# Optimization experiments

Measured on AMD Instinct MI355X. Metric: run time of the kernel, lower is better.

The kernel has to match this reference:

```python
import jax, jax.numpy as jnp
import numpy as np

NP_, NA_ = 100000, 50000           # paper / author node counts
E_C, E_W, E_B = 200000, 100000, 100000  # cites, writes, written_by edges
IN_DIM, OUT_DIM, H, DK = 256, 256, 8, 32
SLOPE, EPS = 0.2, 1e-5


def leaky(x):
    return jnp.where(x >= 0, x, SLOPE * x)


def seg_softmax(scores, seg, n):
    # softmax over edges grouped by destination node (DGL edge_softmax)
    m = jax.ops.segment_max(scores, seg, num_segments=n)
    e = jnp.exp(scores - m[seg])
    z = jax.ops.segment_sum(e, seg, num_segments=n)
    return e / z[seg]


def setup_inputs() -> dict:
    key = jax.random.key(0)
    k = jax.random.split(key, 14)
    s = 1.0 / np.sqrt(IN_DIM)
    return {
        "h_paper": jax.random.normal(k[0], (NP_, IN_DIM), jnp.float32),
        "h_author": jax.random.normal(k[1], (NA_, IN_DIM), jnp.float32),
        "fc_W": jax.random.normal(k[2], (OUT_DIM, IN_DIM), jnp.float32) * s,
        "fce_W": jax.random.normal(k[3], (OUT_DIM, OUT_DIM), jnp.float32) * s,
        "edge_emb": jax.random.normal(k[4], (3, OUT_DIM), jnp.float32) * 0.1,
        "attn_l": jax.random.normal(k[5], (1, H, DK), jnp.float32) * 0.1,
        "attn_r": jax.random.normal(k[6], (1, H, DK), jnp.float32) * 0.1,
        "attn_e": jax.random.normal(k[7], (1, H, DK), jnp.float32) * 0.1,
        "gamma": jnp.ones((OUT_DIM,), jnp.float32),
        "beta": jnp.zeros((OUT_DIM,), jnp.float32),
        "cites_src": jax.random.randint(k[8], (E_C,), 0, NP_),
        "cites_dst": jax.random.randint(k[9], (E_C,), 0, NP_),
        "writes_src": jax.random.randint(k[10], (E_W,), 0, NA_),
        "writes_dst": jax.random.randint(k[11], (E_W,), 0, NP_),
        "wb_src": jax.random.randint(k[12], (E_B,), 0, NP_),
        "wb_dst": jax.random.randint(k[13], (E_B,), 0, NA_),
    }


def reference(h_paper, h_author, fc_W, fce_W, edge_emb, attn_l, attn_r, attn_e,
              gamma, beta, cites_src, cites_dst, writes_src, writes_dst,
              wb_src, wb_dst):
    # fc projection (dropout = identity at eval)
    hp = (h_paper @ fc_W.T).reshape(-1, H, DK)   # [NP,H,DK]
    ha = (h_author @ fc_W.T).reshape(-1, H, DK)  # [NA,H,DK]
    # relation/edge-type embedding term: [3,H]
    ee = ((edge_emb @ fce_W.T).reshape(-1, H, DK) * attn_e).sum(-1)
    el_p = (hp * attn_l).sum(-1)  # [NP,H]
    er_p = (hp * attn_r).sum(-1)
    el_a = (ha * attn_l).sum(-1)
    er_a = (ha * attn_r).sum(-1)
    # per-edge unnormalized attention, leaky_relu(u_add_v + edge term)
    a_c = leaky(el_p[cites_src] + er_p[cites_dst] + ee[0])   # [E_C,H]
    a_w = leaky(el_a[writes_src] + er_p[writes_dst] + ee[1])  # [E_W,H]
    a_b = leaky(el_p[wb_src] + er_a[wb_dst] + ee[2])          # [E_B,H]
    # global softmax per destination node across all incoming relations
    seg_p = jnp.concatenate([cites_dst, writes_dst])
    attn_p = seg_softmax(jnp.concatenate([a_c, a_w], 0), seg_p, NP_)
    attn_a = seg_softmax(a_b, wb_dst, NA_)
    # weighted scatter-sum aggregation (u_mul_e, sum) with cross_reducer=sum
    ft_p = jnp.concatenate([hp[cites_src], ha[writes_src]], 0)  # [E,H,DK]
    t_p = jax.ops.segment_sum(ft_p * attn_p[:, :, None], seg_p,
                              num_segments=NP_).reshape(NP_, OUT_DIM)
    t_a = jax.ops.segment_sum(hp[wb_src] * attn_a[:, :, None], wb_dst,
                              num_segments=NA_).reshape(NA_, OUT_DIM)

    def ln(x):
        mu = x.mean(-1, keepdims=True)
        v = ((x - mu) ** 2).mean(-1, keepdims=True)
        return (x - mu) / jnp.sqrt(v + EPS) * gamma + beta

    out_p = ln(leaky(t_p + hp.reshape(NP_, OUT_DIM)))
    out_a = ln(leaky(t_a + ha.reshape(NA_, OUT_DIM)))
    return out_p, out_a
```

## Files before the change

kernel.cpp:

```cpp
#include <hip/hip_runtime.h>
#include <hip/hip_bf16.h>

#define NPAPER 100000
#define NAUTH  50000
#define NROWS  150000
#define EC 200000
#define EW 100000
#define EB 100000
#define ETOT 400000
#define DIM 256
#define NH 8
#define SLOPE 0.2f
#define LN_EPS 1e-5f
#define MAXD 32

#define NT 2344
#define PROJ_GRID 512
#define TPB 5

typedef unsigned short u16;
typedef __attribute__((ext_vector_type(8))) short s16x8;
typedef __attribute__((ext_vector_type(4))) float f32x4;

__device__ __forceinline__ float lrelu(float x){ return x >= 0.f ? x : SLOPE * x; }
__device__ __forceinline__ u16 f2b(float f){
  __hip_bfloat16 b = __float2bfloat16(f);
  return *reinterpret_cast<u16*>(&b);
}
__device__ __forceinline__ float b2f(u16 u){
  union { unsigned int i; float f; } v; v.i = ((unsigned int)u) << 16; return v.f;
}

__global__ void fill_i32(int* __restrict__ p, int v, int n){
  int i = blockIdx.x * blockDim.x + threadIdx.x;
  int stride = gridDim.x * blockDim.x;
  for (; i < n; i += stride) p[i] = v;
}

__global__ void convert_w(const float4* __restrict__ W4, ushort4* __restrict__ Wb4){
  int i = blockIdx.x * blockDim.x + threadIdx.x;
  float4 v = W4[i];
  ushort4 o; o.x = f2b(v.x); o.y = f2b(v.y); o.z = f2b(v.z); o.w = f2b(v.w);
  Wb4[i] = o;
}

__global__ void ee_kernel(const float* __restrict__ eEmb, const float* __restrict__ fceW,
                          const float* __restrict__ attn_e, float* __restrict__ eew)
{
  const int rel = blockIdx.x / 16;
  const int cg  = blockIdx.x % 16;
  const int wid = threadIdx.x >> 6, l = threadIdx.x & 63;
  const int h = cg >> 1;
  float4 e4 = *reinterpret_cast<const float4*>(eEmb + rel * DIM + l * 4);
  float acc = 0.f;
  #pragma unroll
  for (int cc = 0; cc < 4; cc++){
    int c = cg * 16 + wid * 4 + cc;
    float4 w4 = *reinterpret_cast<const float4*>(fceW + (size_t)c * DIM + l * 4);
    float d = w4.x*e4.x + w4.y*e4.y + w4.z*e4.z + w4.w*e4.w;
    acc += d * attn_e[c];
  }
  #pragma unroll
  for (int m = 32; m > 0; m >>= 1) acc += __shfl_xor(acc, m, 64);
  if (l == 0) atomicAdd(&eew[rel * NH + h], acc);
}

__global__ __launch_bounds__(512) void proj_mfma(
    const float* __restrict__ hP, const float* __restrict__ hA,
    const u16* __restrict__ Wb, u16* __restrict__ out)
{
  const int tid = threadIdx.x;
  const int l = tid & 63, wid = tid >> 6;
  const int lrow = l & 15, g = l >> 4;
  __shared__ u16 xs[2][64 * 256];

  const int t0 = blockIdx.x * TPB;
  if (t0 >= NT) return;
  const int nt = min(TPB, NT - t0);

  s16x8 bW0[8], bW1[8];
  {
    const u16* b0 = Wb + (size_t)(32 * wid + lrow) * DIM + g * 8;
    const u16* b1 = b0 + 16 * DIM;
    #pragma unroll
    for (int k = 0; k < 8; k++){
      bW0[k] = *reinterpret_cast<const s16x8*>(b0 + k * 32);
      bW1[k] = *reinterpret_cast<const s16x8*>(b1 + k * 32);
    }
  }

  float4 v[8];
  #pragma unroll
  for (int it = 0; it < 8; it++){
    int i = tid + it * 512;
    int row = i >> 6, c4 = (i & 63) << 2;
    int gr = t0 * 64 + row; gr = gr < NROWS ? gr : NROWS - 1;
    const float* base = (gr < NPAPER) ? hP + (size_t)gr * DIM + c4
                                      : hA + (size_t)(gr - NPAPER) * DIM + c4;
    v[it] = *reinterpret_cast<const float4*>(base);
  }
  #pragma unroll
  for (int it = 0; it < 8; it++){
    int i = tid + it * 512;
    int row = i >> 6, c4 = (i & 63) << 2;
    ushort4 o; o.x = f2b(v[it].x); o.y = f2b(v[it].y); o.z = f2b(v[it].z); o.w = f2b(v[it].w);
    int byte = (row * 256 + c4) * 2;
    byte ^= (row & 7) << 4;
    *reinterpret_cast<ushort4*>((char*)&xs[0][0] + byte) = o;
  }
  __syncthreads();

  for (int i = 0; i < nt; i++){
    const int cur = i & 1;
    const bool more = (i + 1 < nt);
    if (more){
      #pragma unroll
      for (int it = 0; it < 8; it++){
        int ii = tid + it * 512;
        int row = ii >> 6, c4 = (ii & 63) << 2;
        int gr = (t0 + i + 1) * 64 + row; gr = gr < NROWS ? gr : NROWS - 1;
        const float* base = (gr < NPAPER) ? hP + (size_t)gr * DIM + c4
                                          : hA + (size_t)(gr - NPAPER) * DIM + c4;
        v[it] = *reinterpret_cast<const float4*>(base);
      }
    }
    f32x4 acc[4][2];
    #pragma unroll
    for (int mi = 0; mi < 4; mi++){
      acc[mi][0] = (f32x4){0.f,0.f,0.f,0.f};
      acc[mi][1] = (f32x4){0.f,0.f,0.f,0.f};
    }
    #pragma unroll
    for (int kk = 0; kk < 8; kk++){
      s16x8 aF[4];
      #pragma unroll
      for (int mi = 0; mi < 4; mi++){
        int row = mi * 16 + lrow;
        int byte = (row * 256 + kk * 32 + g * 8) * 2;
        byte ^= (row & 7) << 4;
        aF[mi] = *reinterpret_cast<const s16x8*>((const char*)&xs[cur][0] + byte);
      }
      #pragma unroll
      for (int mi = 0; mi < 4; mi++){
        acc[mi][0] = __builtin_amdgcn_mfma_f32_16x16x32_bf16(aF[mi], bW0[kk], acc[mi][0], 0, 0, 0);
        acc[mi][1] = __builtin_amdgcn_mfma_f32_16x16x32_bf16(aF[mi], bW1[kk], acc[mi][1], 0, 0, 0);
      }
    }
    {
      int r0 = (t0 + i) * 64;
      #pragma unroll
      for (int mi = 0; mi < 4; mi++){
        int rbase = r0 + mi * 16 + g * 4;
        #pragma unroll
        for (int ni = 0; ni < 2; ni++){
          int col = 32 * wid + ni * 16 + lrow;
          #pragma unroll
          for (int reg = 0; reg < 4; reg++){
            int r = rbase + reg;
            if (r < NROWS)
              out[(size_t)r * DIM + col] = f2b(ni ? acc[mi][1][reg] : acc[mi][0][reg]);
          }
        }
      }
    }
    if (more){
      #pragma unroll
      for (int it = 0; it < 8; it++){
        int ii = tid + it * 512;
        int row = ii >> 6, c4 = (ii & 63) << 2;
        ushort4 o; o.x = f2b(v[it].x); o.y = f2b(v[it].y); o.z = f2b(v[it].z); o.w = f2b(v[it].w);
        int byte = (row * 256 + c4) * 2;
        byte ^= (row & 7) << 4;
        *reinterpret_cast<ushort4*>((char*)&xs[1 - cur][0] + byte) = o;
      }
    }
    __syncthreads();
  }
}

__global__ __launch_bounds__(256) void elr_kernel(const u16* __restrict__ hprojb,
    const float* __restrict__ attn_l, const float* __restrict__ attn_r,
    float* __restrict__ el, float* __restrict__ er)
{
  const int wid = threadIdx.x >> 6, l = threadIdx.x & 63;
  const int row = blockIdx.x * 4 + wid;
  if (row >= NROWS) return;
  ushort4 u = *reinterpret_cast<const ushort4*>(hprojb + (size_t)row * DIM + l * 4);
  float v0 = b2f(u.x), v1 = b2f(u.y), v2 = b2f(u.z), v3 = b2f(u.w);
  float4 al = *reinterpret_cast<const float4*>(attn_l + l * 4);
  float4 ar = *reinterpret_cast<const float4*>(attn_r + l * 4);
  float sl = v0*al.x + v1*al.y + v2*al.z + v3*al.w;
  float sr = v0*ar.x + v1*ar.y + v2*ar.z + v3*ar.w;
  #pragma unroll
  for (int m = 1; m < 8; m <<= 1){
    sl += __shfl_xor(sl, m, 64);
    sr += __shfl_xor(sr, m, 64);
  }
  if ((l & 7) == 0){
    int h = l >> 3;
    el[(size_t)row*NH+h] = sl;
    er[(size_t)row*NH+h] = sr;
  }
}

__global__ void scatter_direct(const int* __restrict__ c_src, const int* __restrict__ c_dst,
                               const int* __restrict__ w_src, const int* __restrict__ w_dst,
                               const int* __restrict__ b_src, const int* __restrict__ b_dst,
                               int* __restrict__ cursor, int* __restrict__ eidx){
  int i = blockIdx.x * blockDim.x + threadIdx.x;
  int gd, pk;
  if (i < EC)           { gd = c_dst[i];                pk = c_src[i]; }
  else if (i < EC + EW) { gd = w_dst[i - EC];           pk = (w_src[i - EC] + NPAPER) | (1 << 20); }
  else if (i < ETOT)    { gd = NPAPER + b_dst[i - EC - EW]; pk = b_src[i - EC - EW] | (2 << 20); }
  else return;
  int pos = atomicAdd(&cursor[gd], 1);
  if (pos < MAXD) eidx[(size_t)gd * MAXD + pos] = pk;
}

template<int K>
__device__ __forceinline__ void proc_edges(
    const int* __restrict__ erow, int base, int cnt,
    const float* __restrict__ el, float er_h,
    float ee0, float ee1, float ee2,
    const u16* __restrict__ hprojb, int l, int h,
    float& ax, float& ay, float& az, float& aw, float& zl)
{
  int pk[K]; float w[K]; ushort4 u[K];
  #pragma unroll
  for (int j = 0; j < K; j++)
    pk[j] = erow[base + (j < cnt ? j : 0)];
  #pragma unroll
  for (int j = 0; j < K; j++){
    int gs = pk[j] & 0xFFFFF, rl = pk[j] >> 20;
    u[j] = *reinterpret_cast<const ushort4*>(hprojb + (size_t)gs * DIM + l * 4);
    float sc = el[(size_t)gs * NH + h] + er_h + (rl == 0 ? ee0 : (rl == 1 ? ee1 : ee2));
    w[j] = (j < cnt) ? __expf(lrelu(sc)) : 0.f;
  }
  #pragma unroll
  for (int j = 0; j < K; j++){
    zl += w[j];
    ax += w[j] * b2f(u[j].x); ay += w[j] * b2f(u[j].y);
    az += w[j] * b2f(u[j].z); aw += w[j] * b2f(u[j].w);
  }
}

__global__ __launch_bounds__(256) void agg_ln_kernel(
    const int* __restrict__ counts, const int* __restrict__ eidx,
    const u16* __restrict__ hprojb,
    const float* __restrict__ el, const float* __restrict__ er,
    const float* __restrict__ eew, const float* __restrict__ gamma,
    const float* __restrict__ beta, float* __restrict__ out)
{
  const int wid = threadIdx.x >> 6, l = threadIdx.x & 63;
  const int r = blockIdx.x * 4 + wid;
  if (r >= NROWS) return;
  const int h = l >> 3;
  const float er_h = er[(size_t)r * NH + h];
  const float ee0 = eew[h], ee1 = eew[NH + h], ee2 = eew[2*NH + h];
  const int deg = min(counts[r], MAXD);
  const int* erow = eidx + (size_t)r * MAXD;

  float ax = 0.f, ay = 0.f, az = 0.f, aw = 0.f, zl = 0.f;
  int base = 0;
  while (deg - base >= 8){
    proc_edges<8>(erow, base, 8, el, er_h, ee0, ee1, ee2, hprojb, l, h, ax, ay, az, aw, zl);
    base += 8;
  }
  int rem = deg - base;
  if (rem > 4)      proc_edges<8>(erow, base, rem, el, er_h, ee0, ee1, ee2, hprojb, l, h, ax, ay, az, aw, zl);
  else if (rem > 2) proc_edges<4>(erow, base, rem, el, er_h, ee0, ee1, ee2, hprojb, l, h, ax, ay, az, aw, zl);
  else if (rem > 0) proc_edges<2>(erow, base, rem, el, er_h, ee0, ee1, ee2, hprojb, l, h, ax, ay, az, aw, zl);

  float iz = (deg > 0) ? 1.f / zl : 0.f;
  ushort4 hr = *reinterpret_cast<const ushort4*>(hprojb + (size_t)r * DIM + l * 4);
  float x0 = lrelu(ax * iz + b2f(hr.x));
  float x1 = lrelu(ay * iz + b2f(hr.y));
  float x2 = lrelu(az * iz + b2f(hr.z));
  float x3 = lrelu(aw * iz + b2f(hr.w));
  float s = x0 + x1 + x2 + x3;
  float q = x0*x0 + x1*x1 + x2*x2 + x3*x3;
  #pragma unroll
  for (int m = 32; m > 0; m >>= 1){
    s += __shfl_xor(s, m, 64);
    q += __shfl_xor(q, m, 64);
  }
  float mu  = s * (1.f / DIM);
  float var = q * (1.f / DIM) - mu * mu;
  float inv = rsqrtf(var + LN_EPS);
  float4 g  = *reinterpret_cast<const float4*>(gamma + l * 4);
  float4 bt = *reinterpret_cast<const float4*>(beta + l * 4);
  float4 o;
  o.x = (x0 - mu) * inv * g.x + bt.x;
  o.y = (x1 - mu) * inv * g.y + bt.y;
  o.z = (x2 - mu) * inv * g.z + bt.z;
  o.w = (x3 - mu) * inv * g.w + bt.w;
  *reinterpret_cast<float4*>(out + (size_t)r * DIM + l * 4) = o;
}

extern "C" void kernel_launch(void* const* d_in, const int* in_sizes, int n_in,
                              void* d_out, int out_size, void* d_ws, size_t ws_size,
                              hipStream_t stream)
{
  const float* hP     = (const float*)d_in[0];
  const float* hA     = (const float*)d_in[1];
  const float* fcW    = (const float*)d_in[2];
  const float* fceW   = (const float*)d_in[3];
  const float* eEmb   = (const float*)d_in[4];
  const float* attn_l = (const float*)d_in[5];
  const float* attn_r = (const float*)d_in[6];
  const float* attn_e = (const float*)d_in[7];
  const float* gamma  = (const float*)d_in[8];
  const float* beta   = (const float*)d_in[9];
  const int* c_src  = (const int*)d_in[10];
  const int* c_dst  = (const int*)d_in[11];
  const int* w_src  = (const int*)d_in[12];
  const int* w_dst  = (const int*)d_in[13];
  const int* b_src  = (const int*)d_in[14];
  const int* b_dst  = (const int*)d_in[15];

  u16*   hprojb = (u16*)d_ws;
  float* el    = (float*)(hprojb + (size_t)NROWS * DIM);
  float* er    = el    + (size_t)NROWS * NH;
  float* eew   = er    + (size_t)NROWS * NH;
  int*   cursor= (int*)(eew + 32);
  int*   eidx  = cursor + NROWS;
  u16*   Wb    = (u16*)(eidx + (size_t)NROWS * MAXD);

  const int TB = 256;

  fill_i32<<<256, TB, 0, stream>>>((int*)eew, 0, 32 + NROWS);
  scatter_direct<<<(ETOT + TB - 1) / TB, TB, 0, stream>>>(c_src, c_dst, w_src, w_dst,
                                                          b_src, b_dst, cursor, eidx);

  convert_w<<<64, TB, 0, stream>>>((const float4*)fcW, (ushort4*)Wb);
  ee_kernel<<<48, TB, 0, stream>>>(eEmb, fceW, attn_e, eew);
  proj_mfma<<<PROJ_GRID, 512, 0, stream>>>(hP, hA, Wb, hprojb);
  elr_kernel<<<(NROWS + 3) / 4, TB, 0, stream>>>(hprojb, attn_l, attn_r, el, er);

  agg_ln_kernel<<<NROWS / 4, TB, 0, stream>>>(cursor, eidx, hprojb,
                                              el, er, eew, gamma, beta,
                                              (float*)d_out);
}
```

Baseline: 191.6 us.

## Replace persistent double-buffered projection with one 64-row tile per block

The projection GEMM previously ran as 512 persistent blocks, each handling 5 tiles and overlapping the next tile's global load with the current tile's MFMA work through double-buffered shared memory. It now launches one block per 64-row tile (2344 blocks), each using a single shared buffer, and issues the input load before the weight-fragment load. This halves the shared memory per block so more blocks can be resident and the hardware scheduler can overlap work across blocks. The cost is that every block reloads the weight fragments into registers and there is no explicit software pipelining.

Result: slower. 214.8 us (+12.1%).

```diff
diff --git a/kernel.cpp b/kernel.cpp
--- a/kernel.cpp
+++ b/kernel.cpp
@@ -15,8 +15,6 @@
 #define MAXD 32
 
 #define NT 2344
-#define PROJ_GRID 512
-#define TPB 5
 
 typedef unsigned short u16;
 typedef __attribute__((ext_vector_type(8))) short s16x8;
@@ -72,12 +70,20 @@
   const int tid = threadIdx.x;
   const int l = tid & 63, wid = tid >> 6;
   const int lrow = l & 15, g = l >> 4;
-  __shared__ u16 xs[2][64 * 256];
-
-  const int t0 = blockIdx.x * TPB;
-  if (t0 >= NT) return;
-  const int nt = min(TPB, NT - t0);
-
+  __shared__ u16 xs[64 * 256];
+
+  const int r0 = blockIdx.x * 64;
+
+  float4 v[8];
+  #pragma unroll
+  for (int it = 0; it < 8; it++){
+    int i = tid + it * 512;
+    int row = i >> 6, c4 = (i & 63) << 2;
+    int gr = r0 + row; gr = gr < NROWS ? gr : NROWS - 1;
+    const float* base = (gr < NPAPER) ? hP + (size_t)gr * DIM + c4
+                                      : hA + (size_t)(gr - NPAPER) * DIM + c4;
+    v[it] = *reinterpret_cast<const float4*>(base);
+  }
   s16x8 bW0[8], bW1[8];
   {
     const u16* b0 = Wb + (size_t)(32 * wid + lrow) * DIM + g * 8;
@@ -88,17 +94,6 @@
       bW1[k] = *reinterpret_cast<const s16x8*>(b1 + k * 32);
     }
   }
-
-  float4 v[8];
-  #pragma unroll
-  for (int it = 0; it < 8; it++){
-    int i = tid + it * 512;
-    int row = i >> 6, c4 = (i & 63) << 2;
-    int gr = t0 * 64 + row; gr = gr < NROWS ? gr : NROWS - 1;
-    const float* base = (gr < NPAPER) ? hP + (size_t)gr * DIM + c4
-                                      : hA + (size_t)(gr - NPAPER) * DIM + c4;
-    v[it] = *reinterpret_cast<const float4*>(base);
-  }
   #pragma unroll
   for (int it = 0; it < 8; it++){
     int i = tid + it * 512;
@@ -106,75 +101,46 @@
     ushort4 o; o.x = f2b(v[it].x); o.y = f2b(v[it].y); o.z = f2b(v[it].z); o.w = f2b(v[it].w);
     int byte = (row * 256 + c4) * 2;
     byte ^= (row & 7) << 4;
-    *reinterpret_cast<ushort4*>((char*)&xs[0][0] + byte) = o;
+    *reinterpret_cast<ushort4*>((char*)&xs[0] + byte) = o;
   }
   __syncthreads();
 
-  for (int i = 0; i < nt; i++){
-    const int cur = i & 1;
-    const bool more = (i + 1 < nt);
-    if (more){
+  f32x4 acc[4][2];
+  #pragma unroll
+  for (int mi = 0; mi < 4; mi++){
+    acc[mi][0] = (f32x4){0.f,0.f,0.f,0.f};
+    acc[mi][1] = (f32x4){0.f,0.f,0.f,0.f};
+  }
+  #pragma unroll
+  for (int kk = 0; kk < 8; kk++){
+    s16x8 aF[4];
+    #pragma unroll
+    for (int mi = 0; mi < 4; mi++){
+      int row = mi * 16 + lrow;
+      int byte = (row * 256 + kk * 32 + g * 8) * 2;
+      byte ^= (row & 7) << 4;
+      aF[mi] = *reinterpret_cast<const s16x8*>((const char*)&xs[0] + byte);
+    }
+    #pragma unroll
+    for (int mi = 0; mi < 4; mi++){
+      acc[mi][0] = __builtin_amdgcn_mfma_f32_16x16x32_bf16(aF[mi], bW0[kk], acc[mi][0], 0, 0, 0);
+      acc[mi][1] = __builtin_amdgcn_mfma_f32_16x16x32_bf16(aF[mi], bW1[kk], acc[mi][1], 0, 0, 0);
+    }
+  }
+
+  #pragma unroll
+  for (int mi = 0; mi < 4; mi++){
+    int rbase = r0 + mi * 16 + g * 4;
+    #pragma unroll
+    for (int ni = 0; ni < 2; ni++){
+      int col = 32 * wid + ni * 16 + lrow;
       #pragma unroll
-      for (int it = 0; it < 8; it++){
-        int ii = tid + it * 512;
-        int row = ii >> 6, c4 = (ii & 63) << 2;
-        int gr = (t0 + i + 1) * 64 + row; gr = gr < NROWS ? gr : NROWS - 1;
-        const float* base = (gr < NPAPER) ? hP + (size_t)gr * DIM + c4
-                                          : hA + (size_t)(gr - NPAPER) * DIM + c4;
-        v[it] = *reinterpret_cast<const float4*>(base);
+      for (int reg = 0; reg < 4; reg++){
+        int r = rbase + reg;
+        if (r < NROWS)
+          out[(size_t)r * DIM + col] = f2b(ni ? acc[mi][1][reg] : acc[mi][0][reg]);
       }
     }
-    f32x4 acc[4][2];
-    #pragma unroll
-    for (int mi = 0; mi < 4; mi++){
-      acc[mi][0] = (f32x4){0.f,0.f,0.f,0.f};
-      acc[mi][1] = (f32x4){0.f,0.f,0.f,0.f};
-    }
-    #pragma unroll
-    for (int kk = 0; kk < 8; kk++){
-      s16x8 aF[4];
-      #pragma unroll
-      for (int mi = 0; mi < 4; mi++){
-        int row = mi * 16 + lrow;
-        int byte = (row * 256 + kk * 32 + g * 8) * 2;
-        byte ^= (row & 7) << 4;
-        aF[mi] = *reinterpret_cast<const s16x8*>((const char*)&xs[cur][0] + byte);
-      }
-      #pragma unroll
-      for (int mi = 0; mi < 4; mi++){
-        acc[mi][0] = __builtin_amdgcn_mfma_f32_16x16x32_bf16(aF[mi], bW0[kk], acc[mi][0], 0, 0, 0);
-        acc[mi][1] = __builtin_amdgcn_mfma_f32_16x16x32_bf16(aF[mi], bW1[kk], acc[mi][1], 0, 0, 0);
-      }
-    }
-    {
-      int r0 = (t0 + i) * 64;
-      #pragma unroll
-      for (int mi = 0; mi < 4; mi++){
-        int rbase = r0 + mi * 16 + g * 4;
-        #pragma unroll
-        for (int ni = 0; ni < 2; ni++){
-          int col = 32 * wid + ni * 16 + lrow;
-          #pragma unroll
-          for (int reg = 0; reg < 4; reg++){
-            int r = rbase + reg;
-            if (r < NROWS)
-              out[(size_t)r * DIM + col] = f2b(ni ? acc[mi][1][reg] : acc[mi][0][reg]);
-          }
-        }
-      }
-    }
-    if (more){
-      #pragma unroll
-      for (int it = 0; it < 8; it++){
-        int ii = tid + it * 512;
-        int row = ii >> 6, c4 = (ii & 63) << 2;
-        ushort4 o; o.x = f2b(v[it].x); o.y = f2b(v[it].y); o.z = f2b(v[it].z); o.w = f2b(v[it].w);
-        int byte = (row * 256 + c4) * 2;
-        byte ^= (row & 7) << 4;
-        *reinterpret_cast<ushort4*>((char*)&xs[1 - cur][0] + byte) = o;
-      }
-    }
-    __syncthreads();
   }
 }
 
@@ -334,7 +300,7 @@
 
   convert_w<<<64, TB, 0, stream>>>((const float4*)fcW, (ushort4*)Wb);
   ee_kernel<<<48, TB, 0, stream>>>(eEmb, fceW, attn_e, eew);
-  proj_mfma<<<PROJ_GRID, 512, 0, stream>>>(hP, hA, Wb, hprojb);
+  proj_mfma<<<NT, 512, 0, stream>>>(hP, hA, Wb, hprojb);
   elr_kernel<<<(NROWS + 3) / 4, TB, 0, stream>>>(hprojb, attn_l, attn_r, el, er);
 
   agg_ln_kernel<<<NROWS / 4, TB, 0, stream>>>(cursor, eidx, hprojb,
```

## Fuse attention logit projection into GEMM and stage output through LDS

Applied to the files above, without the earlier changes.

Folds attn_l/attn_r into the fc weight to form a 16-column bf16 matrix (WLRb), so el/er are computed by extra MFMAs in wave 0 of the projection kernel. This removes the separate elr kernel, which re-read the whole projected tensor. The GEMM output is also staged through shared memory for coalesced 16-byte row stores, and the weight conversion and ee kernels are merged into one prep launch. In exchange it adds a barrier per tile, leaves wave 0 with extra MFMA work, and computes el/er from bf16-rounded combined weights rather than from rounded projections.

After: 201.4 us. 5.1% more time.

```diff
diff --git a/kernel.cpp b/kernel.cpp
--- a/kernel.cpp
+++ b/kernel.cpp
@@ -37,37 +37,55 @@
   for (; i < n; i += stride) p[i] = v;
 }
 
-__global__ void convert_w(const float4* __restrict__ W4, ushort4* __restrict__ Wb4){
-  int i = blockIdx.x * blockDim.x + threadIdx.x;
-  float4 v = W4[i];
-  ushort4 o; o.x = f2b(v.x); o.y = f2b(v.y); o.z = f2b(v.z); o.w = f2b(v.w);
-  Wb4[i] = o;
-}
-
-__global__ void ee_kernel(const float* __restrict__ eEmb, const float* __restrict__ fceW,
-                          const float* __restrict__ attn_e, float* __restrict__ eew)
-{
-  const int rel = blockIdx.x / 16;
-  const int cg  = blockIdx.x % 16;
-  const int wid = threadIdx.x >> 6, l = threadIdx.x & 63;
-  const int h = cg >> 1;
-  float4 e4 = *reinterpret_cast<const float4*>(eEmb + rel * DIM + l * 4);
-  float acc = 0.f;
-  #pragma unroll
-  for (int cc = 0; cc < 4; cc++){
-    int c = cg * 16 + wid * 4 + cc;
-    float4 w4 = *reinterpret_cast<const float4*>(fceW + (size_t)c * DIM + l * 4);
-    float d = w4.x*e4.x + w4.y*e4.y + w4.z*e4.z + w4.w*e4.w;
-    acc += d * attn_e[c];
-  }
-  #pragma unroll
-  for (int m = 32; m > 0; m >>= 1) acc += __shfl_xor(acc, m, 64);
-  if (l == 0) atomicAdd(&eew[rel * NH + h], acc);
+__global__ void prep_kernel(const float* __restrict__ fcW, const float* __restrict__ fceW,
+                            const float* __restrict__ eEmb,
+                            const float* __restrict__ attn_l, const float* __restrict__ attn_r,
+                            const float* __restrict__ attn_e,
+                            u16* __restrict__ Wb, u16* __restrict__ WLRb,
+                            float* __restrict__ eew)
+{
+  const int blk = blockIdx.x, tid = threadIdx.x;
+  if (blk < 64){
+    int i = blk * 256 + tid;
+    float4 v = reinterpret_cast<const float4*>(fcW)[i];
+    ushort4 o; o.x = f2b(v.x); o.y = f2b(v.y); o.z = f2b(v.z); o.w = f2b(v.w);
+    reinterpret_cast<ushort4*>(Wb)[i] = o;
+  } else if (blk < 72){
+    int h = blk - 64, k = tid;
+    float sL = 0.f, sR = 0.f;
+    #pragma unroll 8
+    for (int cc = 0; cc < 32; cc++){
+      int c = h * 32 + cc;
+      float wv = fcW[(size_t)c * DIM + k];
+      sL += wv * attn_l[c];
+      sR += wv * attn_r[c];
+    }
+    WLRb[h * DIM + k]       = f2b(sL);
+    WLRb[(8 + h) * DIM + k] = f2b(sR);
+  } else {
+    int b = blk - 72;
+    int rel = b / 16, cg = b % 16;
+    int wid = tid >> 6, l = tid & 63;
+    int h = cg >> 1;
+    float4 e4 = *reinterpret_cast<const float4*>(eEmb + rel * DIM + l * 4);
+    float acc = 0.f;
+    #pragma unroll
+    for (int cc = 0; cc < 4; cc++){
+      int c = cg * 16 + wid * 4 + cc;
+      float4 w4 = *reinterpret_cast<const float4*>(fceW + (size_t)c * DIM + l * 4);
+      float d = w4.x*e4.x + w4.y*e4.y + w4.z*e4.z + w4.w*e4.w;
+      acc += d * attn_e[c];
+    }
+    #pragma unroll
+    for (int m = 32; m > 0; m >>= 1) acc += __shfl_xor(acc, m, 64);
+    if (l == 0) atomicAdd(&eew[rel * NH + h], acc);
+  }
 }
 
 __global__ __launch_bounds__(512) void proj_mfma(
     const float* __restrict__ hP, const float* __restrict__ hA,
-    const u16* __restrict__ Wb, u16* __restrict__ out)
+    const u16* __restrict__ Wb, const u16* __restrict__ WLRb,
+    u16* __restrict__ out, float* __restrict__ el, float* __restrict__ er)
 {
   const int tid = threadIdx.x;
   const int l = tid & 63, wid = tid >> 6;
@@ -78,14 +96,16 @@
   if (t0 >= NT) return;
   const int nt = min(TPB, NT - t0);
 
-  s16x8 bW0[8], bW1[8];
+  s16x8 bW0[8], bW1[8], bE[8];
   {
     const u16* b0 = Wb + (size_t)(32 * wid + lrow) * DIM + g * 8;
     const u16* b1 = b0 + 16 * DIM;
+    const u16* be = WLRb + lrow * DIM + g * 8;
     #pragma unroll
     for (int k = 0; k < 8; k++){
       bW0[k] = *reinterpret_cast<const s16x8*>(b0 + k * 32);
       bW1[k] = *reinterpret_cast<const s16x8*>(b1 + k * 32);
+      bE[k]  = *reinterpret_cast<const s16x8*>(be + k * 32);
     }
   }
 
@@ -113,22 +133,24 @@
   for (int i = 0; i < nt; i++){
     const int cur = i & 1;
     const bool more = (i + 1 < nt);
+    const int r0 = (t0 + i) * 64;
     if (more){
       #pragma unroll
       for (int it = 0; it < 8; it++){
         int ii = tid + it * 512;
         int row = ii >> 6, c4 = (ii & 63) << 2;
-        int gr = (t0 + i + 1) * 64 + row; gr = gr < NROWS ? gr : NROWS - 1;
+        int gr = r0 + 64 + row; gr = gr < NROWS ? gr : NROWS - 1;
         const float* base = (gr < NPAPER) ? hP + (size_t)gr * DIM + c4
                                           : hA + (size_t)(gr - NPAPER) * DIM + c4;
         v[it] = *reinterpret_cast<const float4*>(base);
       }
     }
-    f32x4 acc[4][2];
+    f32x4 acc[4][2], accE[4];
     #pragma unroll
     for (int mi = 0; mi < 4; mi++){
       acc[mi][0] = (f32x4){0.f,0.f,0.f,0.f};
       acc[mi][1] = (f32x4){0.f,0.f,0.f,0.f};
+      accE[mi]   = (f32x4){0.f,0.f,0.f,0.f};
     }
     #pragma unroll
     for (int kk = 0; kk < 8; kk++){
@@ -145,20 +167,36 @@
         acc[mi][0] = __builtin_amdgcn_mfma_f32_16x16x32_bf16(aF[mi], bW0[kk], acc[mi][0], 0, 0, 0);
         acc[mi][1] = __builtin_amdgcn_mfma_f32_16x16x32_bf16(aF[mi], bW1[kk], acc[mi][1], 0, 0, 0);
       }
-    }
-    {
-      int r0 = (t0 + i) * 64;
+      if (wid == 0){
+        #pragma unroll
+        for (int mi = 0; mi < 4; mi++)
+          accE[mi] = __builtin_amdgcn_mfma_f32_16x16x32_bf16(aF[mi], bE[kk], accE[mi], 0, 0, 0);
+      }
+    }
+    __syncthreads();
+
+    #pragma unroll
+    for (int mi = 0; mi < 4; mi++){
+      #pragma unroll
+      for (int ni = 0; ni < 2; ni++){
+        int col = 32 * wid + ni * 16 + lrow;
+        #pragma unroll
+        for (int reg = 0; reg < 4; reg++){
+          int lr = mi * 16 + g * 4 + reg;
+          xs[cur][lr * 256 + col] = f2b(ni ? acc[mi][1][reg] : acc[mi][0][reg]);
+        }
+      }
+    }
+    if (wid == 0){
       #pragma unroll
       for (int mi = 0; mi < 4; mi++){
         int rbase = r0 + mi * 16 + g * 4;
         #pragma unroll
-        for (int ni = 0; ni < 2; ni++){
-          int col = 32 * wid + ni * 16 + lrow;
-          #pragma unroll
-          for (int reg = 0; reg < 4; reg++){
-            int r = rbase + reg;
-            if (r < NROWS)
-              out[(size_t)r * DIM + col] = f2b(ni ? acc[mi][1][reg] : acc[mi][0][reg]);
+        for (int reg = 0; reg < 4; reg++){
+          int r = rbase + reg;
+          if (r < NROWS){
+            if (lrow < 8) el[(size_t)r * NH + lrow]     = accE[mi][reg];
+            else          er[(size_t)r * NH + lrow - 8] = accE[mi][reg];
           }
         }
       }
@@ -175,31 +213,17 @@
       }
     }
     __syncthreads();
-  }
-}
-
-__global__ __launch_bounds__(256) void elr_kernel(const u16* __restrict__ hprojb,
-    const float* __restrict__ attn_l, const float* __restrict__ attn_r,
-    float* __restrict__ el, float* __restrict__ er)
-{
-  const int wid = threadIdx.x >> 6, l = threadIdx.x & 63;
-  const int row = blockIdx.x * 4 + wid;
-  if (row >= NROWS) return;
-  ushort4 u = *reinterpret_cast<const ushort4*>(hprojb + (size_t)row * DIM + l * 4);
-  float v0 = b2f(u.x), v1 = b2f(u.y), v2 = b2f(u.z), v3 = b2f(u.w);
-  float4 al = *reinterpret_cast<const float4*>(attn_l + l * 4);
-  float4 ar = *reinterpret_cast<const float4*>(attn_r + l * 4);
-  float sl = v0*al.x + v1*al.y + v2*al.z + v3*al.w;
-  float sr = v0*ar.x + v1*ar.y + v2*ar.z + v3*ar.w;
-  #pragma unroll
-  for (int m = 1; m < 8; m <<= 1){
-    sl += __shfl_xor(sl, m, 64);
-    sr += __shfl_xor(sr, m, 64);
-  }
-  if ((l & 7) == 0){
-    int h = l >> 3;
-    el[(size_t)row*NH+h] = sl;
-    er[(size_t)row*NH+h] = sr;
+
+    {
+      int lr = tid >> 3, cg16 = (tid & 7) * 32;
+      int grow = r0 + lr;
+      if (grow < NROWS){
+        uint4* dst = reinterpret_cast<uint4*>(out + (size_t)grow * DIM + cg16);
+        const uint4* srcp = reinterpret_cast<const uint4*>(&xs[cur][lr * 256 + cg16]);
+        #pragma unroll
+        for (int j = 0; j < 4; j++) dst[j] = srcp[j];
+      }
+    }
   }
 }
 
@@ -325,6 +349,7 @@
   int*   cursor= (int*)(eew + 32);
   int*   eidx  = cursor + NROWS;
   u16*   Wb    = (u16*)(eidx + (size_t)NROWS * MAXD);
+  u16*   WLRb  = Wb + DIM * DIM;
 
   const int TB = 256;
 
@@ -332,10 +357,9 @@
   scatter_direct<<<(ETOT + TB - 1) / TB, TB, 0, stream>>>(c_src, c_dst, w_src, w_dst,
                                                           b_src, b_dst, cursor, eidx);
 
-  convert_w<<<64, TB, 0, stream>>>((const float4*)fcW, (ushort4*)Wb);
-  ee_kernel<<<48, TB, 0, stream>>>(eEmb, fceW, attn_e, eew);
-  proj_mfma<<<PROJ_GRID, 512, 0, stream>>>(hP, hA, Wb, hprojb);
-  elr_kernel<<<(NROWS + 3) / 4, TB, 0, stream>>>(hprojb, attn_l, attn_r, el, er);
+  prep_kernel<<<120, TB, 0, stream>>>(fcW, fceW, eEmb, attn_l, attn_r, attn_e,
+                                      Wb, WLRb, eew);
+  proj_mfma<<<PROJ_GRID, 512, 0, stream>>>(hP, hA, Wb, WLRb, hprojb, el, er);
 
   agg_ln_kernel<<<NROWS / 4, TB, 0, stream>>>(cursor, eidx, hprojb,
                                               el, er, eew, gamma, beta,
```
